# Kernel optimization log

Hardware: AMD Instinct MI355X
Metric: run time of the kernel (lower is better)

The kernel has to match this reference:

```python
import jax, jax.numpy as jnp
import numpy as np

B, S, D, H, DK, DV = 4, 1024, 1024, 16, 64, 64


def setup_inputs() -> dict:
    key = jax.random.key(0)
    ks = jax.random.split(key, 12)
    sc = 0.02
    return {
        "q": jax.random.normal(ks[0], (B, S, D), jnp.float32),
        "k": jax.random.normal(ks[1], (B, S, D), jnp.float32),
        "v": jax.random.normal(ks[2], (B, S, D), jnp.float32),
        "attn_mask": jax.random.randint(ks[3], (B, S, S), 0, 2).astype(bool),
        "Wq": jax.random.normal(ks[4], (D, H * DK), jnp.float32) * sc,
        "bq": jnp.zeros((H * DK,), jnp.float32),
        "Wk": jax.random.normal(ks[5], (D, H * DK), jnp.float32) * sc,
        "bk": jnp.zeros((H * DK,), jnp.float32),
        "Wv": jax.random.normal(ks[6], (D, H * DV), jnp.float32) * sc,
        "bv": jnp.zeros((H * DV,), jnp.float32),
        "Wo": jax.random.normal(ks[7], (H * DV, D), jnp.float32) * sc,
        "bo": jnp.zeros((D,), jnp.float32),
    }


def _layer_norm(x, eps=1e-5):
    # fresh nn.LayerNorm in forward => weight=1, bias=0
    mu = jnp.mean(x, axis=-1, keepdims=True)
    var = jnp.mean(jnp.square(x - mu), axis=-1, keepdims=True)
    return (x - mu) * jax.lax.rsqrt(var + eps)


def reference(q, k, v, attn_mask, Wq, bq, Wk, bk, Wv, bv, Wo, bo):
    residual = q
    qs = (q @ Wq + bq).reshape(B, S, H, DK).transpose(0, 2, 1, 3)  # [B,H,S,dk]
    ks = (k @ Wk + bk).reshape(B, S, H, DK).transpose(0, 2, 1, 3)
    vs = (v @ Wv + bv).reshape(B, S, H, DV).transpose(0, 2, 1, 3)
    scores = jnp.einsum('bhqd,bhkd->bhqk', qs, ks) / jnp.sqrt(jnp.float32(DK))
    scores = jnp.where(attn_mask[:, None, :, :], jnp.float32(-1e9), scores)
    attention = jax.nn.softmax(scores, axis=-1)  # [B,H,S,S]
    context = jnp.einsum('bhqk,bhkd->bhqd', attention, vs)
    concat = context.transpose(0, 2, 1, 3).reshape(B, S, H * DV)
    output = concat @ Wo + bo
    return _layer_norm(output + residual), attention
```

## Files before the change

kernel.cpp:

```cpp
#include <hip/hip_runtime.h>
#include <hip/hip_bf16.h>
#include <stdint.h>

#define B_    4
#define S_    1024
#define D_    1024
#define H_    16
#define NTOK  4096

typedef __bf16 bf16_t;
typedef bf16_t bf16x8 __attribute__((ext_vector_type(8)));
typedef bf16_t bf16x4 __attribute__((ext_vector_type(4)));
typedef float  f32x4  __attribute__((ext_vector_type(4)));

__device__ __forceinline__ f32x4 mfma16(bf16x8 a, bf16x8 b, f32x4 c) {
  return __builtin_amdgcn_mfma_f32_16x16x32_bf16(a, b, c, 0, 0, 0);
}
__device__ __forceinline__ void gload16(const void* g, void* l) {
  __builtin_amdgcn_global_load_lds((__attribute__((address_space(1))) uint32_t*)g,
                                   (__attribute__((address_space(3))) uint32_t*)l, 16, 0, 0);
}
__device__ __forceinline__ bf16_t to_bf(float x) { return (bf16_t)x; }

__global__ void cvt3_kernel(const float* __restrict__ q, const float* __restrict__ k,
                            const float* __restrict__ v, bf16_t* __restrict__ qb,
                            bf16_t* __restrict__ kb, bf16_t* __restrict__ vb) {
  int z = blockIdx.z;
  const float* src = (z == 0) ? q : ((z == 1) ? k : v);
  bf16_t* dst = (z == 0) ? qb : ((z == 1) ? kb : vb);
  int i = blockIdx.x * blockDim.x + threadIdx.x;
  f32x4 val = ((const f32x4*)src)[i];
  bf16x4 o = { to_bf(val[0]), to_bf(val[1]), to_bf(val[2]), to_bf(val[3]) };
  ((bf16x4*)dst)[i] = o;
}

__global__ void wT4_kernel(const float* __restrict__ Wq, const float* __restrict__ Wk,
                           const float* __restrict__ Wv, const float* __restrict__ Wo,
                           bf16_t* __restrict__ WqT, bf16_t* __restrict__ WkT,
                           bf16_t* __restrict__ WvT, bf16_t* __restrict__ WoT) {
  int z = blockIdx.z;
  const float* W = (z == 0) ? Wq : ((z == 1) ? Wk : ((z == 2) ? Wv : Wo));
  bf16_t* WT = (z == 0) ? WqT : ((z == 1) ? WkT : ((z == 2) ? WvT : WoT));
  __shared__ float t[32][33];
  int bx = blockIdx.x * 32, by = blockIdx.y * 32;
  int tx = threadIdx.x, ty = threadIdx.y;
#pragma unroll
  for (int i = 0; i < 4; i++) t[ty + 8 * i][tx] = W[(size_t)(by + ty + 8 * i) * 1024 + bx + tx];
  __syncthreads();
#pragma unroll
  for (int i = 0; i < 4; i++)
    WT[(size_t)(bx + ty + 8 * i) * 1024 + by + tx] = to_bf(t[tx][ty + 8 * i]);
}

__global__ void maskpack_kernel(const uint32_t* __restrict__ m, uint32_t* __restrict__ out) {
  int t = blockIdx.x * blockDim.x + threadIdx.x;
  const uint32_t* p = m + (size_t)t * 8;
  uint32_t r = 0;
#pragma unroll
  for (int j = 0; j < 8; j++) {
    uint32_t v = p[j];
    uint32_t nib = (v & 1u) | ((v >> 7) & 2u) | ((v >> 14) & 4u) | ((v >> 21) & 8u);
    r |= nib << (j * 4);
  }
  out[t] = r;
}

__device__ __forceinline__ void gemm128_core(const bf16_t* __restrict__ A,
                                             const bf16_t* __restrict__ Bm,
                                             int m0, int n0,
                                             bf16_t* As, bf16_t* Bs, f32x4 (&acc)[4][4]) {
  int tid = threadIdx.x, w = tid >> 6, lane = tid & 63, l16 = lane & 15, lg = lane >> 4;
  int wr = w >> 1, wc = w & 1;
  f32x4 zv = {0.f, 0.f, 0.f, 0.f};
#pragma unroll
  for (int r = 0; r < 4; r++)
#pragma unroll
    for (int c = 0; c < 4; c++) acc[r][c] = zv;

  for (int kt = 0; kt < 16; kt++) {
    int k0 = kt * 64;
#pragma unroll
    for (int j = 0; j < 4; j++) {
      int e = ((w * 4 + j) << 9) + (lane << 3);
      int row = e >> 6, col = e & 63;
      gload16(A + (size_t)(m0 + row) * 1024 + k0 + col, As + ((w * 4 + j) << 9));
      gload16(Bm + (size_t)(n0 + row) * 1024 + k0 + col, Bs + ((w * 4 + j) << 9));
    }
    __syncthreads();
#pragma unroll
    for (int kk = 0; kk < 2; kk++) {
      bf16x8 av[4], bv[4];
#pragma unroll
      for (int r = 0; r < 4; r++)
        av[r] = *(const bf16x8*)(As + (wr * 64 + r * 16 + l16) * 64 + kk * 32 + lg * 8);
#pragma unroll
      for (int c = 0; c < 4; c++)
        bv[c] = *(const bf16x8*)(Bs + (wc * 64 + c * 16 + l16) * 64 + kk * 32 + lg * 8);
#pragma unroll
      for (int r = 0; r < 4; r++)
#pragma unroll
        for (int c = 0; c < 4; c++) acc[r][c] = mfma16(av[r], bv[c], acc[r][c]);
    }
    __syncthreads();
  }
}

__global__ __launch_bounds__(256, 2) void qkv_gemm_kernel(
    const bf16_t* __restrict__ qb, const bf16_t* __restrict__ kb, const bf16_t* __restrict__ vb,
    const bf16_t* __restrict__ WqT, const bf16_t* __restrict__ WkT, const bf16_t* __restrict__ WvT,
    const float* __restrict__ bq, const float* __restrict__ bk, const float* __restrict__ bv,
    bf16_t* __restrict__ Qh, bf16_t* __restrict__ Kh, bf16_t* __restrict__ Vh) {
  __shared__ bf16_t As[128 * 64], Bs[128 * 64];
  int z = blockIdx.z;
  const bf16_t* A  = (z == 0) ? qb  : ((z == 1) ? kb  : vb);
  const bf16_t* Bm = (z == 0) ? WqT : ((z == 1) ? WkT : WvT);
  const float* bias = (z == 0) ? bq : ((z == 1) ? bk : bv);
  bf16_t* out = (z == 0) ? Qh : ((z == 1) ? Kh : Vh);
  int m0 = blockIdx.y * 128, n0 = blockIdx.x * 128;
  f32x4 acc[4][4];
  gemm128_core(A, Bm, m0, n0, As, Bs, acc);

  int tid = threadIdx.x, w = tid >> 6, lane = tid & 63, l16 = lane & 15, lg = lane >> 4;
  int wr = w >> 1, wc = w & 1;
#pragma unroll
  for (int c = 0; c < 4; c++) {
    int col = n0 + wc * 64 + c * 16 + l16;
    float bb = bias[col];
    int h = col >> 6, dk = col & 63;
#pragma unroll
    for (int r = 0; r < 4; r++) {
#pragma unroll
      for (int i = 0; i < 4; i++) {
        int mrow = m0 + wr * 64 + r * 16 + lg * 4 + i;
        int b = mrow >> 10, s = mrow & 1023;
        out[(((size_t)(b * 16 + h)) * 1024 + s) * 64 + dk] = to_bf(acc[r][c][i] + bb);
      }
    }
  }
}

__global__ void vT_kernel(const bf16_t* __restrict__ Vh, bf16_t* __restrict__ Vt) {
  __shared__ float t[64][65];
  int bh = blockIdx.z * 16 + blockIdx.y;
  int s0 = blockIdx.x * 64;
  int tx = threadIdx.x & 63, ty = threadIdx.x >> 6;
  const bf16_t* src = Vh + (size_t)bh * 65536;
  bf16_t* dst = Vt + (size_t)bh * 65536;
#pragma unroll
  for (int i = 0; i < 16; i++) t[ty + 4 * i][tx] = (float)src[(size_t)(s0 + ty + 4 * i) * 64 + tx];
  __syncthreads();
#pragma unroll
  for (int i = 0; i < 16; i++)
    dst[(size_t)(ty + 4 * i) * 1024 + s0 + tx] = to_bf(t[tx][ty + 4 * i]);
}

__global__ __launch_bounds__(256, 2) void attn_kernel(
    const bf16_t* __restrict__ Qh, const bf16_t* __restrict__ Kh, const bf16_t* __restrict__ Vt,
    const uint32_t* __restrict__ mbits, float* __restrict__ attn_out, bf16_t* __restrict__ ctx) {
  constexpr int PSTR = 1032;
  __shared__ bf16_t P[32 * PSTR];
  __shared__ uint32_t mb[1024];
  __shared__ float redm[128], reds[128], rowinv[32];

  int lin = blockIdx.x + 32 * (blockIdx.y + 16 * blockIdx.z);
  int xcd = lin & 7;
  int slot = lin >> 3;
  int bh = xcd * 8 + (slot >> 5);
  int q0 = (slot & 31) * 32;
  int b = bh >> 4;

  int tid = threadIdx.x, w = tid >> 6, lane = tid & 63, l16 = lane & 15, lg = lane >> 4;

  ((uint4*)mb)[tid] = ((const uint4*)(mbits + ((size_t)b * 1024 + q0) * 32))[tid];

  const bf16_t* Qb = Qh + (size_t)bh * 65536;
  const bf16_t* Kb = Kh + (size_t)bh * 65536;
  bf16x8 qa[2][2];
#pragma unroll
  for (int r = 0; r < 2; r++)
#pragma unroll
    for (int kk = 0; kk < 2; kk++)
      qa[r][kk] = *(const bf16x8*)(Qb + (size_t)(q0 + r * 16 + l16) * 64 + kk * 32 + lg * 8);

  f32x4 zv = {0.f, 0.f, 0.f, 0.f};
  f32x4 sc[2][16];
#pragma unroll
  for (int rt = 0; rt < 2; rt++)
#pragma unroll
    for (int c = 0; c < 16; c++) sc[rt][c] = zv;
  int kcol0 = w * 256;
#pragma unroll 4
  for (int c = 0; c < 16; c++) {
#pragma unroll
    for (int kk = 0; kk < 2; kk++) {
      bf16x8 kv = *(const bf16x8*)(Kb + (size_t)(kcol0 + c * 16 + l16) * 64 + kk * 32 + lg * 8);
      sc[0][c] = mfma16(qa[0][kk], kv, sc[0][c]);
      sc[1][c] = mfma16(qa[1][kk], kv, sc[1][c]);
    }
  }
  __syncthreads();

  float rmax[2][4], rsum[2][4], rinv[2][4];
#pragma unroll
  for (int rt = 0; rt < 2; rt++)
#pragma unroll
    for (int i = 0; i < 4; i++) rmax[rt][i] = -3e38f;
  const float scale = 0.125f;
#pragma unroll
  for (int rt = 0; rt < 2; rt++) {
#pragma unroll
    for (int j = 0; j < 8; j++) {
      uint32_t wd[4];
#pragma unroll
      for (int i = 0; i < 4; i++) wd[i] = mb[(rt * 16 + lg * 4 + i) * 32 + w * 8 + j];
#pragma unroll
      for (int hf = 0; hf < 2; hf++) {
        int c = j * 2 + hf;
#pragma unroll
        for (int i = 0; i < 4; i++) {
          float s = sc[rt][c][i] * scale;
          if ((wd[i] >> (l16 + hf * 16)) & 1u) s = -1e9f;
          sc[rt][c][i] = s;
          rmax[rt][i] = fmaxf(rmax[rt][i], s);
        }
      }
    }
  }
#pragma unroll
  for (int m = 1; m < 16; m <<= 1)
#pragma unroll
    for (int rt = 0; rt < 2; rt++)
#pragma unroll
      for (int i = 0; i < 4; i++) rmax[rt][i] = fmaxf(rmax[rt][i], __shfl_xor(rmax[rt][i], m));
  if (l16 == 0) {
#pragma unroll
    for (int rt = 0; rt < 2; rt++)
#pragma unroll
      for (int i = 0; i < 4; i++) redm[w * 32 + rt * 16 + lg * 4 + i] = rmax[rt][i];
  }
  __syncthreads();
#pragma unroll
  for (int rt = 0; rt < 2; rt++)
#pragma unroll
    for (int i = 0; i < 4; i++) {
      int row = rt * 16 + lg * 4 + i;
      rmax[rt][i] = fmaxf(fmaxf(redm[row], redm[32 + row]), fmaxf(redm[64 + row], redm[96 + row]));
      rsum[rt][i] = 0.f;
    }
#pragma unroll
  for (int rt = 0; rt < 2; rt++)
#pragma unroll
    for (int c = 0; c < 16; c++)
#pragma unroll
      for (int i = 0; i < 4; i++) {
        float p = __expf(sc[rt][c][i] - rmax[rt][i]);
        sc[rt][c][i] = p;
        rsum[rt][i] += p;
      }
#pragma unroll
  for (int m = 1; m < 16; m <<= 1)
#pragma unroll
    for (int rt = 0; rt < 2; rt++)
#pragma unroll
      for (int i = 0; i < 4; i++) rsum[rt][i] += __shfl_xor(rsum[rt][i], m);
  if (l16 == 0) {
#pragma unroll
    for (int rt = 0; rt < 2; rt++)
#pragma unroll
      for (int i = 0; i < 4; i++) reds[w * 32 + rt * 16 + lg * 4 + i] = rsum[rt][i];
  }
  __syncthreads();
#pragma unroll
  for (int rt = 0; rt < 2; rt++)
#pragma unroll
    for (int i = 0; i < 4; i++) {
      int row = rt * 16 + lg * 4 + i;
      float gs = reds[row] + reds[32 + row] + reds[64 + row] + reds[96 + row];
      rinv[rt][i] = 1.0f / gs;
    }
  if (w == 0 && l16 == 0) {
#pragma unroll
    for (int rt = 0; rt < 2; rt++)
#pragma unroll
      for (int i = 0; i < 4; i++) rowinv[rt * 16 + lg * 4 + i] = rinv[rt][i];
  }

#pragma unroll
  for (int rt = 0; rt < 2; rt++)
#pragma unroll
    for (int c = 0; c < 16; c++) {
      int colk = kcol0 + c * 16 + l16;
#pragma unroll
      for (int i = 0; i < 4; i++) {
        int row = rt * 16 + lg * 4 + i;
        P[row * PSTR + colk] = to_bf(sc[rt][c][i]);
      }
    }
  __syncthreads();

  f32x4 oacc0 = zv, oacc1 = zv;
  const bf16_t* Vb = Vt + ((size_t)bh * 64 + w * 16 + l16) * 1024 + lg * 8;
#pragma unroll 4
  for (int ks = 0; ks < 32; ks++) {
    bf16x8 vv = *(const bf16x8*)(Vb + ks * 32);
    bf16x8 a0 = *(const bf16x8*)(P + l16 * PSTR + ks * 32 + lg * 8);
    bf16x8 a1 = *(const bf16x8*)(P + (16 + l16) * PSTR + ks * 32 + lg * 8);
    oacc0 = mfma16(a0, vv, oacc0);
    oacc1 = mfma16(a1, vv, oacc1);
  }

  float* ob = attn_out + ((size_t)bh * 1024 + q0) * 1024;
#pragma unroll
  for (int rr = 0; rr < 8; rr++) {
    int row = w * 8 + rr;
    float inv = rowinv[row];
#pragma unroll
    for (int c = 0; c < 4; c++) {
      int col = c * 256 + lane * 4;
      bf16x4 p4 = *(const bf16x4*)(P + row * PSTR + col);
      f32x4 o = { (float)p4[0] * inv, (float)p4[1] * inv, (float)p4[2] * inv, (float)p4[3] * inv };
      __builtin_nontemporal_store(o, (f32x4*)(ob + (size_t)row * 1024 + col));
    }
  }

#pragma unroll
  for (int i = 0; i < 4; i++) {
    int s0r = q0 + lg * 4 + i;
    ctx[((size_t)b * 1024 + s0r) * 1024 + (bh & 15) * 64 + w * 16 + l16] = to_bf(oacc0[i] * rinv[0][i]);
    int s1r = q0 + 16 + lg * 4 + i;
    ctx[((size_t)b * 1024 + s1r) * 1024 + (bh & 15) * 64 + w * 16 + l16] = to_bf(oacc1[i] * rinv[1][i]);
  }
}

__global__ __launch_bounds__(256, 2) void out_gemm_kernel(
    const bf16_t* __restrict__ ctx, const bf16_t* __restrict__ WoT,
    const float* __restrict__ bo, const float* __restrict__ resid, float* __restrict__ preLN) {
  __shared__ bf16_t As[128 * 64], Bs[128 * 64];
  int m0 = blockIdx.y * 128, n0 = blockIdx.x * 128;
  f32x4 acc[4][4];
  gemm128_core(ctx, WoT, m0, n0, As, Bs, acc);
  int tid = threadIdx.x, w = tid >> 6, lane = tid & 63, l16 = lane & 15, lg = lane >> 4;
  int wr = w >> 1, wc = w & 1;
#pragma unroll
  for (int c = 0; c < 4; c++) {
    int col = n0 + wc * 64 + c * 16 + l16;
    float bb = bo[col];
#pragma unroll
    for (int r = 0; r < 4; r++) {
#pragma unroll
      for (int i = 0; i < 4; i++) {
        int mrow = m0 + wr * 64 + r * 16 + lg * 4 + i;
        preLN[(size_t)mrow * 1024 + col] = acc[r][c][i] + bb + resid[(size_t)mrow * 1024 + col];
      }
    }
  }
}

__global__ void ln_kernel(const float* __restrict__ pre, float* __restrict__ out) {
  int row = blockIdx.x, tid = threadIdx.x;
  const f32x4 v = ((const f32x4*)(pre + (size_t)row * 1024))[tid];
  float s = v[0] + v[1] + v[2] + v[3];
  float s2 = v[0] * v[0] + v[1] * v[1] + v[2] * v[2] + v[3] * v[3];
#pragma unroll
  for (int m = 32; m > 0; m >>= 1) { s += __shfl_xor(s, m); s2 += __shfl_xor(s2, m); }
  __shared__ float rs[4], rs2[4];
  int w = tid >> 6;
  if ((tid & 63) == 0) { rs[w] = s; rs2[w] = s2; }
  __syncthreads();
  float S = rs[0] + rs[1] + rs[2] + rs[3];
  float S2 = rs2[0] + rs2[1] + rs2[2] + rs2[3];
  float mu = S * (1.f / 1024.f);
  float var = S2 * (1.f / 1024.f) - mu * mu;
  float rstd = rsqrtf(var + 1e-5f);
  f32x4 o = { (v[0] - mu) * rstd, (v[1] - mu) * rstd, (v[2] - mu) * rstd, (v[3] - mu) * rstd };
  ((f32x4*)(out + (size_t)row * 1024))[tid] = o;
}

extern "C" void kernel_launch(void* const* d_in, const int* in_sizes, int n_in,
                              void* d_out, int out_size, void* d_ws, size_t ws_size,
                              hipStream_t stream) {
  const float* q  = (const float*)d_in[0];
  const float* k  = (const float*)d_in[1];
  const float* v  = (const float*)d_in[2];
  const uint8_t* mask = (const uint8_t*)d_in[3];
  const float* Wq = (const float*)d_in[4];
  const float* bq = (const float*)d_in[5];
  const float* Wk = (const float*)d_in[6];
  const float* bk = (const float*)d_in[7];
  const float* Wv = (const float*)d_in[8];
  const float* bv = (const float*)d_in[9];
  const float* Wo = (const float*)d_in[10];
  const float* bo = (const float*)d_in[11];

  char* wsp = (char*)d_ws;
  size_t off = 0;
  auto carve = [&](size_t bytes) { void* p = wsp + off; off += (bytes + 255) & ~(size_t)255; return p; };
  bf16_t* qb  = (bf16_t*)carve((size_t)NTOK * 1024 * 2);
  bf16_t* kb  = (bf16_t*)carve((size_t)NTOK * 1024 * 2);
  bf16_t* vb  = (bf16_t*)carve((size_t)NTOK * 1024 * 2);
  bf16_t* WqT = (bf16_t*)carve((size_t)1024 * 1024 * 2);
  bf16_t* WkT = (bf16_t*)carve((size_t)1024 * 1024 * 2);
  bf16_t* WvT = (bf16_t*)carve((size_t)1024 * 1024 * 2);
  bf16_t* WoT = (bf16_t*)carve((size_t)1024 * 1024 * 2);
  bf16_t* Qh  = (bf16_t*)carve((size_t)NTOK * 1024 * 2);
  bf16_t* Kh  = (bf16_t*)carve((size_t)NTOK * 1024 * 2);
  bf16_t* Vh  = (bf16_t*)carve((size_t)NTOK * 1024 * 2);
  bf16_t* Vt  = (bf16_t*)carve((size_t)NTOK * 1024 * 2);
  bf16_t* ctx = (bf16_t*)carve((size_t)NTOK * 1024 * 2);
  uint32_t* mbits = (uint32_t*)carve((size_t)B_ * S_ * 32 * 4);
  float* preLN = (float*)carve((size_t)NTOK * 1024 * 4);
  (void)ws_size; (void)in_sizes; (void)n_in; (void)out_size;

  float* lnout = (float*)d_out;
  float* attn_out = (float*)d_out + (size_t)NTOK * 1024;

  cvt3_kernel<<<dim3(4096, 1, 3), 256, 0, stream>>>(q, k, v, qb, kb, vb);
  wT4_kernel<<<dim3(32, 32, 4), dim3(32, 8), 0, stream>>>(Wq, Wk, Wv, Wo, WqT, WkT, WvT, WoT);
  maskpack_kernel<<<512, 256, 0, stream>>>((const uint32_t*)mask, mbits);
  qkv_gemm_kernel<<<dim3(8, 32, 3), 256, 0, stream>>>(qb, kb, vb, WqT, WkT, WvT,
                                                      bq, bk, bv, Qh, Kh, Vh);
  vT_kernel<<<dim3(16, 16, 4), 256, 0, stream>>>(Vh, Vt);
  attn_kernel<<<dim3(32, 16, 4), 256, 0, stream>>>(Qh, Kh, Vt, mbits, attn_out, ctx);
  out_gemm_kernel<<<dim3(8, 32), 256, 0, stream>>>(ctx, WoT, bo, q, preLN);
  ln_kernel<<<4096, 256, 0, stream>>>(preLN, lnout);
}
```

Before: 722.5 us.

## Drop LDS P buffer; stage normalized probabilities through output attention tensor

The QKV projection now writes token-major [B,S,H*dk] output instead of head-major, and the attention and V-transpose kernels index that layout directly. The attention kernel no longer keeps a 64KB LDS probability tile. It writes normalized fp32 probabilities straight from registers to the attention output, waits for those stores, then reads them back from global memory as the A operand for the PV MFMA. The launch-bounds occupancy hint is also removed. Freeing LDS could raise occupancy, but the kernel now does scattered uncoalesced fp32 global stores plus a global re-read of the probabilities, and it relies on a block barrier to make other waves' global writes visible.

```diff
diff --git a/kernel.cpp b/kernel.cpp
--- a/kernel.cpp
+++ b/kernel.cpp
@@ -126,14 +126,12 @@
   for (int c = 0; c < 4; c++) {
     int col = n0 + wc * 64 + c * 16 + l16;
     float bb = bias[col];
-    int h = col >> 6, dk = col & 63;
 #pragma unroll
     for (int r = 0; r < 4; r++) {
 #pragma unroll
       for (int i = 0; i < 4; i++) {
         int mrow = m0 + wr * 64 + r * 16 + lg * 4 + i;
-        int b = mrow >> 10, s = mrow & 1023;
-        out[(((size_t)(b * 16 + h)) * 1024 + s) * 64 + dk] = to_bf(acc[r][c][i] + bb);
+        out[(size_t)mrow * 1024 + col] = to_bf(acc[r][c][i] + bb);
       }
     }
   }
@@ -142,45 +140,43 @@
 __global__ void vT_kernel(const bf16_t* __restrict__ Vh, bf16_t* __restrict__ Vt) {
   __shared__ float t[64][65];
   int bh = blockIdx.z * 16 + blockIdx.y;
+  int b = blockIdx.z, h = blockIdx.y;
   int s0 = blockIdx.x * 64;
   int tx = threadIdx.x & 63, ty = threadIdx.x >> 6;
-  const bf16_t* src = Vh + (size_t)bh * 65536;
   bf16_t* dst = Vt + (size_t)bh * 65536;
 #pragma unroll
-  for (int i = 0; i < 16; i++) t[ty + 4 * i][tx] = (float)src[(size_t)(s0 + ty + 4 * i) * 64 + tx];
+  for (int i = 0; i < 16; i++)
+    t[ty + 4 * i][tx] = (float)Vh[(size_t)(b * 1024 + s0 + ty + 4 * i) * 1024 + h * 64 + tx];
   __syncthreads();
 #pragma unroll
   for (int i = 0; i < 16; i++)
     dst[(size_t)(ty + 4 * i) * 1024 + s0 + tx] = to_bf(t[tx][ty + 4 * i]);
 }
 
-__global__ __launch_bounds__(256, 2) void attn_kernel(
+__global__ __launch_bounds__(256) void attn_kernel(
     const bf16_t* __restrict__ Qh, const bf16_t* __restrict__ Kh, const bf16_t* __restrict__ Vt,
     const uint32_t* __restrict__ mbits, float* __restrict__ attn_out, bf16_t* __restrict__ ctx) {
-  constexpr int PSTR = 1032;
-  __shared__ bf16_t P[32 * PSTR];
   __shared__ uint32_t mb[1024];
-  __shared__ float redm[128], reds[128], rowinv[32];
+  __shared__ float redm[128], reds[128];
 
   int lin = blockIdx.x + 32 * (blockIdx.y + 16 * blockIdx.z);
   int xcd = lin & 7;
   int slot = lin >> 3;
   int bh = xcd * 8 + (slot >> 5);
   int q0 = (slot & 31) * 32;
-  int b = bh >> 4;
+  int b = bh >> 4, h = bh & 15;
 
   int tid = threadIdx.x, w = tid >> 6, lane = tid & 63, l16 = lane & 15, lg = lane >> 4;
 
   ((uint4*)mb)[tid] = ((const uint4*)(mbits + ((size_t)b * 1024 + q0) * 32))[tid];
 
-  const bf16_t* Qb = Qh + (size_t)bh * 65536;
-  const bf16_t* Kb = Kh + (size_t)bh * 65536;
   bf16x8 qa[2][2];
 #pragma unroll
   for (int r = 0; r < 2; r++)
 #pragma unroll
     for (int kk = 0; kk < 2; kk++)
-      qa[r][kk] = *(const bf16x8*)(Qb + (size_t)(q0 + r * 16 + l16) * 64 + kk * 32 + lg * 8);
+      qa[r][kk] = *(const bf16x8*)(Qh + (size_t)(b * 1024 + q0 + r * 16 + l16) * 1024 +
+                                   h * 64 + kk * 32 + lg * 8);
 
   f32x4 zv = {0.f, 0.f, 0.f, 0.f};
   f32x4 sc[2][16];
@@ -193,7 +189,8 @@
   for (int c = 0; c < 16; c++) {
 #pragma unroll
     for (int kk = 0; kk < 2; kk++) {
-      bf16x8 kv = *(const bf16x8*)(Kb + (size_t)(kcol0 + c * 16 + l16) * 64 + kk * 32 + lg * 8);
+      bf16x8 kv = *(const bf16x8*)(Kh + (size_t)(b * 1024 + kcol0 + c * 16 + l16) * 1024 +
+                                   h * 64 + kk * 32 + lg * 8);
       sc[0][c] = mfma16(qa[0][kk], kv, sc[0][c]);
       sc[1][c] = mfma16(qa[1][kk], kv, sc[1][c]);
     }
@@ -278,13 +275,8 @@
       float gs = reds[row] + reds[32 + row] + reds[64 + row] + reds[96 + row];
       rinv[rt][i] = 1.0f / gs;
     }
-  if (w == 0 && l16 == 0) {
-#pragma unroll
-    for (int rt = 0; rt < 2; rt++)
-#pragma unroll
-      for (int i = 0; i < 4; i++) rowinv[rt * 16 + lg * 4 + i] = rinv[rt][i];
-  }
-
+
+  float* ob = attn_out + ((size_t)bh * 1024 + q0) * 1024;
 #pragma unroll
   for (int rt = 0; rt < 2; rt++)
 #pragma unroll
@@ -293,42 +285,34 @@
 #pragma unroll
       for (int i = 0; i < 4; i++) {
         int row = rt * 16 + lg * 4 + i;
-        P[row * PSTR + colk] = to_bf(sc[rt][c][i]);
+        ob[(size_t)row * 1024 + colk] = sc[rt][c][i] * rinv[rt][i];
       }
     }
+  asm volatile("s_waitcnt vmcnt(0)" ::: "memory");
   __syncthreads();
 
   f32x4 oacc0 = zv, oacc1 = zv;
   const bf16_t* Vb = Vt + ((size_t)bh * 64 + w * 16 + l16) * 1024 + lg * 8;
+  const float* prow0 = ob + (size_t)l16 * 1024 + lg * 8;
+  const float* prow1 = ob + (size_t)(16 + l16) * 1024 + lg * 8;
 #pragma unroll 4
   for (int ks = 0; ks < 32; ks++) {
     bf16x8 vv = *(const bf16x8*)(Vb + ks * 32);
-    bf16x8 a0 = *(const bf16x8*)(P + l16 * PSTR + ks * 32 + lg * 8);
-    bf16x8 a1 = *(const bf16x8*)(P + (16 + l16) * PSTR + ks * 32 + lg * 8);
+    f32x4 x0 = *(const f32x4*)(prow0 + ks * 32);
+    f32x4 x1 = *(const f32x4*)(prow0 + ks * 32 + 4);
+    f32x4 y0 = *(const f32x4*)(prow1 + ks * 32);
+    f32x4 y1 = *(const f32x4*)(prow1 + ks * 32 + 4);
+    bf16x8 a0 = { to_bf(x0[0]), to_bf(x0[1]), to_bf(x0[2]), to_bf(x0[3]),
+                  to_bf(x1[0]), to_bf(x1[1]), to_bf(x1[2]), to_bf(x1[3]) };
+    bf16x8 a1 = { to_bf(y0[0]), to_bf(y0[1]), to_bf(y0[2]), to_bf(y0[3]),
+                  to_bf(y1[0]), to_bf(y1[1]), to_bf(y1[2]), to_bf(y1[3]) };
     oacc0 = mfma16(a0, vv, oacc0);
     oacc1 = mfma16(a1, vv, oacc1);
   }
-
-  float* ob = attn_out + ((size_t)bh * 1024 + q0) * 1024;
-#pragma unroll
-  for (int rr = 0; rr < 8; rr++) {
-    int row = w * 8 + rr;
-    float inv = rowinv[row];
-#pragma unroll
-    for (int c = 0; c < 4; c++) {
-      int col = c * 256 + lane * 4;
-      bf16x4 p4 = *(const bf16x4*)(P + row * PSTR + col);
-      f32x4 o = { (float)p4[0] * inv, (float)p4[1] * inv, (float)p4[2] * inv, (float)p4[3] * inv };
-      __builtin_nontemporal_store(o, (f32x4*)(ob + (size_t)row * 1024 + col));
-    }
-  }
-
 #pragma unroll
   for (int i = 0; i < 4; i++) {
-    int s0r = q0 + lg * 4 + i;
-    ctx[((size_t)b * 1024 + s0r) * 1024 + (bh & 15) * 64 + w * 16 + l16] = to_bf(oacc0[i] * rinv[0][i]);
-    int s1r = q0 + 16 + lg * 4 + i;
-    ctx[((size_t)b * 1024 + s1r) * 1024 + (bh & 15) * 64 + w * 16 + l16] = to_bf(oacc1[i] * rinv[1][i]);
+    ctx[(size_t)(b * 1024 + q0 + lg * 4 + i) * 1024 + h * 64 + w * 16 + l16] = to_bf(oacc0[i]);
+    ctx[(size_t)(b * 1024 + q0 + 16 + lg * 4 + i) * 1024 + h * 64 + w * 16 + l16] = to_bf(oacc1[i]);
   }
 }
 
```

New measurement: 885.7 us. 1.23x slower.
